# Kernel optimization log

Measured on AMD Instinct MI355X. Metric: run time of the kernel, lower is better.

The kernel has to match this reference:

```python
import jax, jax.numpy as jnp
import numpy as np

B, H, S, DH = 1, 16, 4096, 64
SPARSITY = 0.1
NEG = -1e9


def setup_inputs() -> dict:
    key = jax.random.key(0)
    kq, kk, kv, kp, km = jax.random.split(key, 5)
    query = jax.random.normal(kq, (B, H, S, DH), dtype=jnp.float32)
    k_ = jax.random.normal(kk, (B, H, S, DH), dtype=jnp.float32)
    v_ = jax.random.normal(kv, (B, H, S, DH), dtype=jnp.float32)
    pat = jax.random.uniform(kp, (S, S)) < SPARSITY
    pat = pat | jnp.eye(S, dtype=bool)
    sparse_pattern = pat[None, None]  # [1,1,S,S]
    mask = jax.random.randint(km, (1, 1, 1, S), 0, 2, dtype=jnp.int32)
    return {"query": query, "key": k_, "value": v_,
            "sparse_pattern": sparse_pattern, "mask": mask}


def reference(query, key, value, sparse_pattern, mask):
    scale = 1.0 / jnp.sqrt(jnp.asarray(DH, dtype=query.dtype))
    # [B,H,S,S] attention scores
    scores = jnp.einsum('bhqd,bhkd->bhqk', query, key) * scale
    scores = jnp.where(sparse_pattern, scores, NEG)
    scores = jnp.where(mask == 0, NEG, scores)
    weights = jax.nn.softmax(scores, axis=-1)
    return jnp.einsum('bhqk,bhkd->bhqd', weights, value)
```

## Files before the change

kernel.cpp:

```cpp
#include <hip/hip_runtime.h>
#include <hip/hip_bf16.h>

#define S_LEN 4096
#define DHD   64
#define NH    16
#define NKT   64
#define KVB   64
#define WQ    32
#define NW    4
#define QB    (WQ * NW)
#define QSCALE 0.18033688011112042f
#define THRS   8.656170245333781f

#if __has_builtin(__builtin_amdgcn_exp2f)
#define EXP2(x) __builtin_amdgcn_exp2f(x)
#else
#define EXP2(x) exp2f(x)
#endif

typedef __bf16 bf16x8 __attribute__((ext_vector_type(8)));
typedef __bf16 bf16x4 __attribute__((ext_vector_type(4)));
typedef float  f32x16 __attribute__((ext_vector_type(16)));
typedef float  f32x4  __attribute__((ext_vector_type(4)));
typedef unsigned u32;
typedef unsigned u32x4v __attribute__((ext_vector_type(4)));
typedef unsigned long long u64;

#define MFMA32 __builtin_amdgcn_mfma_f32_32x32x16_bf16

__device__ __forceinline__ int swz(int row, int col) {
  return row * 64 + ((((col >> 3) ^ (row & 7)) << 3) | (col & 7));
}

__device__ __forceinline__ u32 pk(float a, float b) {
  __bf16 x = (__bf16)a, y = (__bf16)b;
  u32 lo = (u32)__builtin_bit_cast(unsigned short, x);
  u32 hi = (u32)__builtin_bit_cast(unsigned short, y);
  return lo | (hi << 16);
}

__device__ __forceinline__ void gload16(const void* g, void* l) {
  __builtin_amdgcn_global_load_lds((const __attribute__((address_space(1))) void*)g,
                                   (__attribute__((address_space(3))) void*)l, 16, 0, 0);
}

__device__ __forceinline__ void plswap(u32& x, u32& y) {
  asm("v_permlane32_swap_b32 %0, %1" : "+v"(x), "+v"(y));
}

union PAW { u32x4v w; bf16x8 h; };

template <int MODE>
__device__ __forceinline__ bool patget(const void* __restrict__ p, int q, int k) {
  const size_t idx = (size_t)q * S_LEN + k;
  if constexpr (MODE == 1) return ((const unsigned char*)p)[idx] != 0;
  else if constexpr (MODE == 0) return ((const int*)p)[idx] != 0;
  else return ((const float*)p)[idx] != 0.0f;
}

__global__ void __launch_bounds__(256, 2) attn32c(
    const float* __restrict__ Qg, const __bf16* __restrict__ Kc, const __bf16* __restrict__ Vc,
    const u64* __restrict__ packw,
    const int* __restrict__ mask, float* __restrict__ out) {
  __shared__ __align__(16) __bf16 Kls[4][KVB * DHD];
  __shared__ __align__(16) __bf16 Vls[4][DHD * KVB];
  __shared__ float sfb[NW][WQ];
  __shared__ int msum[NW];

  const int gid = (blockIdx.x & 7) * 64 + (blockIdx.x >> 3);
  const int h = gid >> 5;
  const int q0 = (gid & 31) * QB;

  const int t = threadIdx.x, lane = t & 63, wv = t >> 6;
  const int l32 = lane & 31, hi = lane >> 5;
  const int qrow = q0 + wv * WQ + l32;

  int c = 0;
#pragma unroll
  for (int j = 0; j < 16; j++) c += (mask[t * 16 + j] != 0);
#pragma unroll
  for (int d = 1; d < 64; d <<= 1) c += __shfl_xor(c, d);
  if (lane == 0) msum[wv] = c;

  bf16x8 aQ[4];
  {
    const float* qp = Qg + ((size_t)h * S_LEN + qrow) * DHD;
#pragma unroll
    for (int cc = 0; cc < 4; cc++) {
      float4 x = *(const float4*)(qp + cc * 16 + hi * 8);
      float4 y = *(const float4*)(qp + cc * 16 + hi * 8 + 4);
      bf16x8 f;
      f[0] = (__bf16)(x.x * QSCALE); f[1] = (__bf16)(x.y * QSCALE);
      f[2] = (__bf16)(x.z * QSCALE); f[3] = (__bf16)(x.w * QSCALE);
      f[4] = (__bf16)(y.x * QSCALE); f[5] = (__bf16)(y.y * QSCALE);
      f[6] = (__bf16)(y.z * QSCALE); f[7] = (__bf16)(y.w * QSCALE);
      aQ[cc] = f;
    }
  }
  bf16x8 onesf;
#pragma unroll
  for (int j = 0; j < 8; j++) onesf[j] = (__bf16)1.0f;
  f32x16 zv;
#pragma unroll
  for (int r = 0; r < 16; r++) zv[r] = 0.f;

  __syncthreads();
  const int nact = msum[0] + msum[1] + msum[2] + msum[3];
  const int nt = (nact + 63) >> 6;
  const int np = ((nt + 1) & ~1) >> 1;

  const __bf16* Kb = Kc + (size_t)h * NKT * 4096;
  const __bf16* Vb = Vc + (size_t)h * NKT * 4096;

  auto stage = [&](int slot, int kt) {
    const __bf16* kbase = Kb + (size_t)kt * 4096;
    const __bf16* vbase = Vb + (size_t)kt * 4096;
#pragma unroll
    for (int i = 0; i < 2; i++) {
      const int j = wv * 2 + i;
      gload16(kbase + j * 512 + lane * 8, &Kls[slot][j * 512]);
      gload16(vbase + j * 512 + lane * 8, &Vls[slot][j * 512]);
    }
  };

  f32x16 Oc0 = zv, Oc1 = zv, Ol = zv;
  float m_run = -__builtin_inff();
  const u64* prow = packw + qrow;

  __builtin_amdgcn_sched_barrier(0);
  u64 pwA = prow[0];
  u64 pwB = prow[(size_t)1 * S_LEN];
  stage(0, 0);
  stage(1, 1);

  for (int it = 0; it < np; it++) {
    const int buf = (it & 1) << 1;
    u64 pwA_n = 0, pwB_n = 0;
    if (it + 1 < np) {
      pwA_n = prow[(size_t)(2 * it + 2) * S_LEN];
      pwB_n = prow[(size_t)(2 * it + 3) * S_LEN];
      stage(buf ^ 2, 2 * it + 2);
      stage((buf ^ 2) + 1, 2 * it + 3);
      asm volatile("s_waitcnt vmcnt(10)" ::: "memory");
    } else {
      asm volatile("s_waitcnt vmcnt(0)" ::: "memory");
    }
    __builtin_amdgcn_s_barrier();
    __builtin_amdgcn_sched_barrier(0);

    const __bf16* KlA = Kls[buf];
    const __bf16* KlB = Kls[buf + 1];
    const __bf16* VlA = Vls[buf];
    const __bf16* VlB = Vls[buf + 1];

    f32x16 pA0, pA1, pB0, pB1;
    __builtin_amdgcn_s_setprio(1);
#pragma unroll
    for (int cc = 0; cc < 4; cc++) {
      const int g = (((2 * cc + hi) ^ (l32 & 7)) << 3);
      const bf16x8 kA0 = *(const bf16x8*)&KlA[l32 * 64 + g];
      const bf16x8 kA1 = *(const bf16x8*)&KlA[(32 + l32) * 64 + g];
      const bf16x8 kB0 = *(const bf16x8*)&KlB[l32 * 64 + g];
      const bf16x8 kB1 = *(const bf16x8*)&KlB[(32 + l32) * 64 + g];
      pA0 = MFMA32(kA0, aQ[cc], cc ? pA0 : zv, 0, 0, 0);
      pA1 = MFMA32(kA1, aQ[cc], cc ? pA1 : zv, 0, 0, 0);
      pB0 = MFMA32(kB0, aQ[cc], cc ? pB0 : zv, 0, 0, 0);
      pB1 = MFMA32(kB1, aQ[cc], cc ? pB1 : zv, 0, 0, 0);
    }
    __builtin_amdgcn_s_setprio(0);

    float mx[32];
#pragma unroll
    for (int i = 0; i < 8; i++) {
      mx[i]      = fmaxf(pA0[2 * i], pA0[2 * i + 1]);
      mx[8 + i]  = fmaxf(pA1[2 * i], pA1[2 * i + 1]);
      mx[16 + i] = fmaxf(pB0[2 * i], pB0[2 * i + 1]);
      mx[24 + i] = fmaxf(pB1[2 * i], pB1[2 * i + 1]);
    }
#pragma unroll
    for (int s = 16; s >= 1; s >>= 1)
#pragma unroll
      for (int i = 0; i < s; i++) mx[i] = fmaxf(mx[i], mx[i + s]);
    const float pm = fmaxf(mx[0], __shfl_xor(mx[0], 32));

    if (!__all(pm <= m_run + THRS)) {
      const float mn = fmaxf(m_run, pm);
      const float sf = EXP2(m_run - mn);
      m_run = mn;
      if (lane < 32) sfb[wv][l32] = sf;
#pragma unroll
      for (int rq = 0; rq < 4; rq++) {
        const f32x4 s4 = *(const f32x4*)&sfb[wv][rq * 8 + 4 * hi];
#pragma unroll
        for (int rr = 0; rr < 4; rr++) {
          Oc0[rq * 4 + rr] *= s4[rr];
          Oc1[rq * 4 + rr] *= s4[rr];
          Ol[rq * 4 + rr]  *= s4[rr];
        }
      }
    }

    const u32 a0b = (u32)pwA, a1b = (u32)(pwA >> 32);
    const u32 wA0 = hi ? ((a0b >> 4) | (a1b << 28)) : a0b;
    const u32 wA1 = hi ? (a1b >> 4) : a1b;
    const u32 b0b = (u32)pwB, b1b = (u32)(pwB >> 32);
    const u32 wB0 = hi ? ((b0b >> 4) | (b1b << 28)) : b0b;
    const u32 wB1 = hi ? (b1b >> 4) : b1b;

#pragma unroll
    for (int r = 0; r < 16; r++) {
      const int sp = (r & 3) + 8 * (r >> 2);
      float eA0 = EXP2(pA0[r] - m_run);
      float eA1 = EXP2(pA1[r] - m_run);
      float eB0 = EXP2(pB0[r] - m_run);
      float eB1 = EXP2(pB1[r] - m_run);
      const int tA0 = (int)(wA0 << (31 - sp)) >> 31;
      const int tA1 = (int)(wA1 << (31 - sp)) >> 31;
      const int tB0 = (int)(wB0 << (31 - sp)) >> 31;
      const int tB1 = (int)(wB1 << (31 - sp)) >> 31;
      pA0[r] = __uint_as_float(__float_as_uint(eA0) & (u32)tA0);
      pA1[r] = __uint_as_float(__float_as_uint(eA1) & (u32)tA1);
      pB0[r] = __uint_as_float(__float_as_uint(eB0) & (u32)tB0);
      pB1[r] = __uint_as_float(__float_as_uint(eB1) & (u32)tB1);
    }

    __builtin_amdgcn_s_setprio(1);
#pragma unroll
    for (int ks = 0; ks < 4; ks++) {
      const f32x16& ps = (ks < 2) ? pA0 : pA1;
      const int b = (ks & 1) * 8;
      u32 x0 = pk(ps[b + 0], ps[b + 1]), x1 = pk(ps[b + 2], ps[b + 3]);
      u32 y0 = pk(ps[b + 4], ps[b + 5]), y1 = pk(ps[b + 6], ps[b + 7]);
      plswap(x0, y0);
      plswap(x1, y1);
      PAW pa;
      pa.w = (u32x4v){x0, x1, y0, y1};
      const int g = (((2 * ks + hi) ^ (l32 & 7)) << 3);
      const bf16x8 v0 = *(const bf16x8*)&VlA[l32 * 64 + g];
      const bf16x8 v1 = *(const bf16x8*)&VlA[(32 + l32) * 64 + g];
      Oc0 = MFMA32(pa.h, v0, Oc0, 0, 0, 0);
      Oc1 = MFMA32(pa.h, v1, Oc1, 0, 0, 0);
      Ol  = MFMA32(pa.h, onesf, Ol, 0, 0, 0);
    }
#pragma unroll
    for (int ks = 0; ks < 4; ks++) {
      const f32x16& ps = (ks < 2) ? pB0 : pB1;
      const int b = (ks & 1) * 8;
      u32 x0 = pk(ps[b + 0], ps[b + 1]), x1 = pk(ps[b + 2], ps[b + 3]);
      u32 y0 = pk(ps[b + 4], ps[b + 5]), y1 = pk(ps[b + 6], ps[b + 7]);
      plswap(x0, y0);
      plswap(x1, y1);
      PAW pa;
      pa.w = (u32x4v){x0, x1, y0, y1};
      const int g = (((2 * ks + hi) ^ (l32 & 7)) << 3);
      const bf16x8 v0 = *(const bf16x8*)&VlB[l32 * 64 + g];
      const bf16x8 v1 = *(const bf16x8*)&VlB[(32 + l32) * 64 + g];
      Oc0 = MFMA32(pa.h, v0, Oc0, 0, 0, 0);
      Oc1 = MFMA32(pa.h, v1, Oc1, 0, 0, 0);
      Ol  = MFMA32(pa.h, onesf, Ol, 0, 0, 0);
    }
    __builtin_amdgcn_s_setprio(0);

    __builtin_amdgcn_s_barrier();
    pwA = pwA_n;
    pwB = pwB_n;
  }

  float* ob = out + ((size_t)h * S_LEN + q0 + wv * WQ) * DHD;
#pragma unroll
  for (int rq = 0; rq < 4; rq++) {
#pragma unroll
    for (int rr = 0; rr < 4; rr++) {
      const int r = rq * 4 + rr;
      const float linv = 1.0f / Ol[r];
      const int qq = rr + 8 * rq + 4 * hi;
      ob[(size_t)qq * DHD + l32]      = Oc0[r] * linv;
      ob[(size_t)qq * DHD + 32 + l32] = Oc1[r] * linv;
    }
  }
}

__global__ void __launch_bounds__(256) prep_all(
    const unsigned* __restrict__ pat32, const int* __restrict__ mask,
    const float* __restrict__ K, const float* __restrict__ V,
    u64* __restrict__ packw, __bf16* __restrict__ Kc, __bf16* __restrict__ Vc) {
  __shared__ int idxs[S_LEN];
  __shared__ int red8[8];
  __shared__ __align__(16) unsigned rowbuf[4096];
  const int t = threadIdx.x, lane = t & 63, wv = t >> 6;

  unsigned mb = 0;
#pragma unroll
  for (int j = 0; j < 16; j++) mb |= (unsigned)(mask[t * 16 + j] != 0) << j;
  const int cnt = __builtin_popcount(mb);
  int inc = cnt;
  for (int d = 1; d < 64; d <<= 1) {
    const int v = __shfl_up(inc, d);
    if (lane >= d) inc += v;
  }
  if (lane == 63) red8[wv] = inc;
  __syncthreads();
  int base = 0;
  for (int w = 0; w < wv; w++) base += red8[w];
  const int nact = red8[0] + red8[1] + red8[2] + red8[3];
  int pfx = base + inc - cnt;
#pragma unroll
  for (int j = 0; j < 16; j++)
    if ((mb >> j) & 1) idxs[pfx++] = t * 16 + j;
  __syncthreads();
  const int nt = (nact + 63) >> 6;
  const int nte = (nt + 1) & ~1;

  if (blockIdx.x < S_LEN) {
    const int q = blockIdx.x;
    unsigned acc = 0;
    for (int i = t; i < 4096; i += 256) {
      const unsigned w = pat32[i];
      if (w == 0x3F800000u) acc |= 2u;
      else if (w & 0xFFFFFF00u) acc |= 1u;
    }
    for (int d = 1; d < 64; d <<= 1) acc |= (unsigned)__shfl_xor((int)acc, d);
    if (lane == 0) red8[4 + wv] = (int)acc;
    __syncthreads();
    acc = (unsigned)(red8[4] | red8[5] | red8[6] | red8[7]);
    const int mode = (acc & 2u) ? 2 : ((acc & 1u) ? 1 : 0);

    if (mode == 1) {
      const uint4* src = (const uint4*)((const unsigned char*)pat32 + ((size_t)q << 12));
      ((uint4*)rowbuf)[t] = src[t];
    } else {
      const uint4* src = (const uint4*)(pat32 + ((size_t)q << 12));
#pragma unroll
      for (int i = 0; i < 4; i++) ((uint4*)rowbuf)[t + 256 * i] = src[t + 256 * i];
    }
    __syncthreads();
    const unsigned char* rb = (const unsigned char*)rowbuf;
    const int nkw = nte * 64;
    for (int bs = 0; bs < nkw; bs += 256) {
      const int j = bs + t;
      bool pb = false;
      if (j < nact) {
        const int k = idxs[j];
        pb = (mode == 1) ? (rb[k] != 0) : (rowbuf[k] != 0);
      }
      const u64 b = __ballot(pb);
      if ((t & 63) == 0) packw[(size_t)(j >> 6) * S_LEN + q] = b;
    }
  } else {
    const int bb = blockIdx.x - S_LEN;
    const int kt = bb & 63, h = bb >> 6;
    if (kt >= nte) return;
    __bf16* Kd = Kc + ((size_t)(h * NKT + kt)) * 4096;
    __bf16* Vd = Vc + ((size_t)(h * NKT + kt)) * 4096;
    const float* Kb = K + (size_t)h * S_LEN * DHD;
    const float* Vb = V + (size_t)h * S_LEN * DHD;
#pragma unroll
    for (int i = 0; i < 4; i++) {
      const int u = t + 256 * i;
      const int kk = u >> 4, d = (u & 15) * 4;
      const int kg = kt * 64 + kk;
      float4 v = {0.f, 0.f, 0.f, 0.f};
      if (kg < nact) v = *(const float4*)(Kb + (size_t)idxs[kg] * DHD + d);
      bf16x4 b;
      b[0] = (__bf16)v.x; b[1] = (__bf16)v.y; b[2] = (__bf16)v.z; b[3] = (__bf16)v.w;
      *(bf16x4*)&Kd[swz(kk, d)] = b;
    }
#pragma unroll
    for (int i = 0; i < 2; i++) {
      const int u = t + 256 * i;
      const int kp = u & 31, d4 = u >> 5;
      const int g0 = kt * 64 + 2 * kp, g1 = g0 + 1;
      float4 a = {0.f, 0.f, 0.f, 0.f}, b = {0.f, 0.f, 0.f, 0.f};
      if (g0 < nact) a = *(const float4*)(Vb + (size_t)idxs[g0] * DHD + d4 * 4);
      if (g1 < nact) b = *(const float4*)(Vb + (size_t)idxs[g1] * DHD + d4 * 4);
      const float* A = reinterpret_cast<const float*>(&a);
      const float* B = reinterpret_cast<const float*>(&b);
#pragma unroll
      for (int j = 0; j < 4; j++) {
        *(u32*)&Vd[swz(d4 * 4 + j, 2 * kp)] = pk(A[j], B[j]);
      }
    }
  }
}

template <bool PACKED, int MODE>
__global__ void __launch_bounds__(256, 2) attn32(
    const float* __restrict__ Qg, const float* __restrict__ Kg, const float* __restrict__ Vg,
    const u64* __restrict__ packw, const void* __restrict__ pat, const int* __restrict__ mask,
    float* __restrict__ out) {
  __shared__ __align__(16) __bf16 Kls[2][KVB * DHD];
  __shared__ __align__(16) __bf16 Vls[2][DHD * KVB];
  __shared__ float sfb[NW][WQ];
  const int gid = (blockIdx.x & 7) * 64 + (blockIdx.x >> 3);
  const int h = gid >> 5;
  const int q0 = (gid & 31) * QB;
  const int t = threadIdx.x, lane = t & 63, wv = t >> 6;
  const int l32 = lane & 31, hi = lane >> 5;
  const int qrow = q0 + wv * WQ + l32;
  bf16x8 aQ[4];
  {
    const float* qp = Qg + ((size_t)h * S_LEN + qrow) * DHD;
#pragma unroll
    for (int cc = 0; cc < 4; cc++) {
      float4 x = *(const float4*)(qp + cc * 16 + hi * 8);
      float4 y = *(const float4*)(qp + cc * 16 + hi * 8 + 4);
      bf16x8 f;
      f[0] = (__bf16)(x.x * QSCALE); f[1] = (__bf16)(x.y * QSCALE);
      f[2] = (__bf16)(x.z * QSCALE); f[3] = (__bf16)(x.w * QSCALE);
      f[4] = (__bf16)(y.x * QSCALE); f[5] = (__bf16)(y.y * QSCALE);
      f[6] = (__bf16)(y.z * QSCALE); f[7] = (__bf16)(y.w * QSCALE);
      aQ[cc] = f;
    }
  }
  const float* Kb = Kg + (size_t)h * S_LEN * DHD;
  const float* Vb = Vg + (size_t)h * S_LEN * DHD;
  float4 kreg[4], vreg0[2], vreg1[2];
  auto issue_loads = [&](int kt) {
    const float* kbase = Kb + (size_t)kt * KVB * DHD;
    const float* vbase = Vb + (size_t)kt * KVB * DHD;
#pragma unroll
    for (int i = 0; i < 4; i++) {
      const int u = t + 256 * i;
      kreg[i] = *(const float4*)(kbase + (size_t)(u >> 4) * DHD + (u & 15) * 4);
    }
#pragma unroll
    for (int i = 0; i < 2; i++) {
      const int u = t + 256 * i;
      const int kp = u & 31, d4 = u >> 5;
      vreg0[i] = *(const float4*)(vbase + (size_t)(2 * kp) * DHD + d4 * 4);
      vreg1[i] = *(const float4*)(vbase + (size_t)(2 * kp + 1) * DHD + d4 * 4);
    }
  };
  auto write_tile = [&](int buf) {
    __bf16* Kd = Kls[buf];
    __bf16* Vd = Vls[buf];
#pragma unroll
    for (int i = 0; i < 4; i++) {
      const int u = t + 256 * i;
      const int kk = u >> 4, d = (u & 15) * 4;
      const float4 v = kreg[i];
      bf16x4 b;
      b[0] = (__bf16)v.x; b[1] = (__bf16)v.y; b[2] = (__bf16)v.z; b[3] = (__bf16)v.w;
      *(bf16x4*)&Kd[swz(kk, d)] = b;
    }
#pragma unroll
    for (int i = 0; i < 2; i++) {
      const int u = t + 256 * i;
      const int kp = u & 31, d4 = u >> 5;
      const float* A = reinterpret_cast<const float*>(&vreg0[i]);
      const float* B = reinterpret_cast<const float*>(&vreg1[i]);
#pragma unroll
      for (int j = 0; j < 4; j++) {
        *(u32*)&Vd[swz(d4 * 4 + j, 2 * kp)] = pk(A[j], B[j]);
      }
    }
  };
  f32x16 Oc0, Oc1;
#pragma unroll
  for (int r = 0; r < 16; r++) { Oc0[r] = 0.f; Oc1[r] = 0.f; }
  float m_run = -__builtin_inff(), l_run = 0.f;
  const u64* prow = PACKED ? (packw + qrow) : nullptr;
  issue_loads(0);
  write_tile(0);
  __syncthreads();
  int cur = 0;
  for (int kt = 0; kt < NKT; kt++) {
    if (kt + 1 < NKT) issue_loads(kt + 1);
    u64 pw;
    if constexpr (PACKED) {
      pw = prow[(size_t)kt * S_LEN];
    } else {
      pw = 0;
      for (int j = 0; j < 64; j++) {
        const bool pb = patget<MODE>(pat, qrow, kt * 64 + j) && (mask[kt * 64 + j] != 0);
        pw |= (u64)pb << j;
      }
    }
    const __bf16* Kl = Kls[cur];
    f32x16 p0, p1;
#pragma unroll
    for (int r = 0; r < 16; r++) { p0[r] = 0.f; p1[r] = 0.f; }
#pragma unroll
    for (int cc = 0; cc < 4; cc++) {
      const int g = (((2 * cc + hi) ^ (l32 & 7)) << 3);
      const bf16x8 k0 = *(const bf16x8*)&Kl[l32 * 64 + g];
      const bf16x8 k1 = *(const bf16x8*)&Kl[(32 + l32) * 64 + g];
      p0 = MFMA32(k0, aQ[cc], p0, 0, 0, 0);
      p1 = MFMA32(k1, aQ[cc], p1, 0, 0, 0);
    }
    float pm = p0[0];
#pragma unroll
    for (int r = 1; r < 16; r++) pm = fmaxf(pm, p0[r]);
#pragma unroll
    for (int r = 0; r < 16; r++) pm = fmaxf(pm, p1[r]);
    pm = fmaxf(pm, __shfl_xor(pm, 32));
    if (!__all(pm <= m_run + THRS)) {
      const float mn = fmaxf(m_run, pm);
      const float sf = EXP2(m_run - mn);
      m_run = mn;
      l_run *= sf;
      if (lane < 32) sfb[wv][l32] = sf;
#pragma unroll
      for (int rq = 0; rq < 4; rq++) {
        const f32x4 s4 = *(const f32x4*)&sfb[wv][rq * 8 + 4 * hi];
#pragma unroll
        for (int rr = 0; rr < 4; rr++) {
          Oc0[rq * 4 + rr] *= s4[rr];
          Oc1[rq * 4 + rr] *= s4[rr];
        }
      }
    }
    const u32 b0 = (u32)pw, b1 = (u32)(pw >> 32);
    const u32 w0 = hi ? ((b0 >> 4) | (b1 << 28)) : b0;
    const u32 w1 = hi ? (b1 >> 4) : b1;
    float ls = 0.f;
#pragma unroll
    for (int r = 0; r < 16; r++) {
      const int sp = (r & 3) + 8 * (r >> 2);
      float e0 = EXP2(p0[r] - m_run);
      float e1 = EXP2(p1[r] - m_run);
      const int t0 = (int)(w0 << (31 - sp)) >> 31;
      const int t1 = (int)(w1 << (31 - sp)) >> 31;
      e0 = __uint_as_float(__float_as_uint(e0) & (u32)t0);
      e1 = __uint_as_float(__float_as_uint(e1) & (u32)t1);
      p0[r] = e0; p1[r] = e1;
      ls += e0 + e1;
    }
    ls += __shfl_xor(ls, 32);
    l_run += ls;
    const __bf16* Vl = Vls[cur];
#pragma unroll
    for (int ks = 0; ks < 4; ks++) {
      const f32x16& ps = (ks < 2) ? p0 : p1;
      const int b = (ks & 1) * 8;
      u32 x0 = pk(ps[b + 0], ps[b + 1]), x1 = pk(ps[b + 2], ps[b + 3]);
      u32 y0 = pk(ps[b + 4], ps[b + 5]), y1 = pk(ps[b + 6], ps[b + 7]);
      plswap(x0, y0);
      plswap(x1, y1);
      PAW pa;
      pa.w = (u32x4v){x0, x1, y0, y1};
      const int g = (((2 * ks + hi) ^ (l32 & 7)) << 3);
      const bf16x8 v0 = *(const bf16x8*)&Vl[l32 * 64 + g];
      const bf16x8 v1 = *(const bf16x8*)&Vl[(32 + l32) * 64 + g];
      Oc0 = MFMA32(pa.h, v0, Oc0, 0, 0, 0);
      Oc1 = MFMA32(pa.h, v1, Oc1, 0, 0, 0);
    }
    if (kt + 1 < NKT) write_tile(cur ^ 1);
    __syncthreads();
    cur ^= 1;
  }
  const float linv = 1.0f / l_run;
  if (lane < 32) sfb[wv][l32] = linv;
  __syncthreads();
  float* ob = out + ((size_t)h * S_LEN + q0 + wv * WQ) * DHD;
#pragma unroll
  for (int rq = 0; rq < 4; rq++) {
    const f32x4 s4 = *(const f32x4*)&sfb[wv][rq * 8 + 4 * hi];
#pragma unroll
    for (int rr = 0; rr < 4; rr++) {
      const int r = rq * 4 + rr;
      const int qq = rr + 8 * rq + 4 * hi;
      ob[(size_t)qq * DHD + l32]      = Oc0[r] * s4[rr];
      ob[(size_t)qq * DHD + 32 + l32] = Oc1[r] * s4[rr];
    }
  }
}

__global__ void detect_kernel(const unsigned* __restrict__ p, int* __restrict__ flag) {
  __shared__ unsigned red[256];
  const int t = threadIdx.x;
  unsigned acc = 0;
  for (int i = t; i < 16384; i += 256) {
    const unsigned w = p[i];
    if (w == 0x3F800000u) acc |= 2u;
    else if (w & 0xFFFFFF00u) acc |= 1u;
  }
  red[t] = acc;
  __syncthreads();
  if (t == 0) {
    unsigned a = 0;
    for (int i = 0; i < 256; i++) a |= red[i];
    flag[0] = (a & 2u) ? 2 : ((a & 1u) ? 1 : 0);
  }
}

__global__ void pack_mask_kernel(const int* __restrict__ mask, u64* __restrict__ maskw) {
  const int w = threadIdx.x;
  u64 m = 0;
  for (int j = 0; j < 64; j++) m |= (u64)(mask[(w << 6) + j] != 0) << j;
  maskw[w] = m;
}

__global__ void pack_pat_kernel(const void* __restrict__ pat, const u64* __restrict__ maskw,
                                u64* __restrict__ packw, const int* __restrict__ flagp) {
  const int gid = blockIdx.x * 256 + threadIdx.x;
  const int q = gid >> 6, w = gid & 63;
  const int mode = flagp[0];
  u64 bits = 0;
  if (mode == 1) {
    const u64* p = (const u64*)((const unsigned char*)pat + ((size_t)q << 12) + (w << 6));
#pragma unroll
    for (int c = 0; c < 8; c++) {
      u64 v = p[c];
      v |= v >> 4; v |= v >> 2; v |= v >> 1;
      v &= 0x0101010101010101ull;
      bits |= ((v * 0x0102040810204080ull) >> 56) << (c * 8);
    }
  } else if (mode == 0) {
    const int4* p = (const int4*)((const int*)pat + ((size_t)q << 12) + ((size_t)w << 6));
#pragma unroll
    for (int c = 0; c < 16; c++) {
      const int4 x = p[c];
      bits |= (u64)(x.x != 0) << (c * 4);
      bits |= (u64)(x.y != 0) << (c * 4 + 1);
      bits |= (u64)(x.z != 0) << (c * 4 + 2);
      bits |= (u64)(x.w != 0) << (c * 4 + 3);
    }
  } else {
    const float4* p = (const float4*)((const float*)pat + ((size_t)q << 12) + ((size_t)w << 6));
#pragma unroll
    for (int c = 0; c < 16; c++) {
      const float4 x = p[c];
      bits |= (u64)(x.x != 0.0f) << (c * 4);
      bits |= (u64)(x.y != 0.0f) << (c * 4 + 1);
      bits |= (u64)(x.z != 0.0f) << (c * 4 + 2);
      bits |= (u64)(x.w != 0.0f) << (c * 4 + 3);
    }
  }
  packw[(size_t)w * S_LEN + q] = bits & maskw[w];
}

extern "C" void kernel_launch(void* const* d_in, const int* in_sizes, int n_in,
                              void* d_out, int out_size, void* d_ws, size_t ws_size,
                              hipStream_t stream) {
  (void)in_sizes; (void)n_in; (void)out_size;
  const float* Q  = (const float*)d_in[0];
  const float* K  = (const float*)d_in[1];
  const float* V  = (const float*)d_in[2];
  const void* pat = d_in[3];
  const int* mask = (const int*)d_in[4];
  float* out      = (float*)d_out;

  const size_t FLAG_OFF  = 0;
  const size_t MASKW_OFF = 24576;
  const size_t PACKW_OFF = 32768;
  const size_t KC_OFF    = PACKW_OFF + (size_t)S_LEN * NKT * 8;
  const size_t VC_OFF    = KC_OFF + (size_t)NH * NKT * 4096 * 2;
  const size_t NEED_FULL = VC_OFF + (size_t)NH * NKT * 4096 * 2;
  const size_t NEED_MID  = PACKW_OFF + (size_t)S_LEN * NKT * 8;

  const dim3 grid(32 * NH, 1);

  if (ws_size >= NEED_FULL) {
    u64* packw = (u64*)((char*)d_ws + PACKW_OFF);
    __bf16* Kc = (__bf16*)((char*)d_ws + KC_OFF);
    __bf16* Vc = (__bf16*)((char*)d_ws + VC_OFF);
    prep_all<<<S_LEN + NKT * NH, 256, 0, stream>>>((const unsigned*)pat, mask, K, V,
                                                   packw, Kc, Vc);
    attn32c<<<grid, 256, 0, stream>>>(Q, Kc, Vc, packw, mask, out);
  } else if (ws_size >= NEED_MID) {
    int* flag  = (int*)((char*)d_ws + FLAG_OFF);
    u64* maskw = (u64*)((char*)d_ws + MASKW_OFF);
    u64* packw = (u64*)((char*)d_ws + PACKW_OFF);
    detect_kernel<<<1, 256, 0, stream>>>((const unsigned*)pat, flag);
    pack_mask_kernel<<<1, 64, 0, stream>>>(mask, maskw);
    pack_pat_kernel<<<(S_LEN * 64) / 256, 256, 0, stream>>>(pat, maskw, packw, flag);
    attn32<true, 0><<<grid, 256, 0, stream>>>(Q, K, V, packw, pat, mask, out);
  } else {
    attn32<false, 1><<<grid, 256, 0, stream>>>(Q, K, V, nullptr, pat, mask, out);
  }
}
```

Measured before the change: 95.40 us.

## Split KV tiles across two wave groups per block with LDS merge

The attention kernel now launches 512 threads per block. The eight waves form two groups of four, each processing alternating KV tiles for the same 128 query rows with its own double buffer. At the end, group 1 writes its partial O, row sums and running max to shared memory, and group 0 merges them with max-rescaling before the final normalisation. This doubles wave-level parallelism per query block to hide latency and shortens each wave's serial KV loop. The cost is an extra LDS reduction, higher register and LDS pressure (launch bounds now ask for 512 threads and 4 waves per EU), and less work per iteration to overlap loads.

```diff
diff --git a/kernel.cpp b/kernel.cpp
--- a/kernel.cpp
+++ b/kernel.cpp
@@ -7,8 +7,7 @@
 #define NKT   64
 #define KVB   64
 #define WQ    32
-#define NW    4
-#define QB    (WQ * NW)
+#define QB    128
 #define QSCALE 0.18033688011112042f
 #define THRS   8.656170245333781f
 
@@ -58,26 +57,28 @@
   else return ((const float*)p)[idx] != 0.0f;
 }
 
-__global__ void __launch_bounds__(256, 2) attn32c(
+__global__ void __launch_bounds__(512, 4) attn32c(
     const float* __restrict__ Qg, const __bf16* __restrict__ Kc, const __bf16* __restrict__ Vc,
     const u64* __restrict__ packw,
     const int* __restrict__ mask, float* __restrict__ out) {
-  __shared__ __align__(16) __bf16 Kls[4][KVB * DHD];
-  __shared__ __align__(16) __bf16 Vls[4][DHD * KVB];
-  __shared__ float sfb[NW][WQ];
-  __shared__ int msum[NW];
+  __shared__ __align__(16) char smem[65536];
+  __shared__ float sfb[8][WQ];
+  __shared__ int msum[8];
+  __bf16* Kls = (__bf16*)smem;
+  __bf16* Vls = (__bf16*)(smem + 32768);
 
   const int gid = (blockIdx.x & 7) * 64 + (blockIdx.x >> 3);
   const int h = gid >> 5;
   const int q0 = (gid & 31) * QB;
 
   const int t = threadIdx.x, lane = t & 63, wv = t >> 6;
+  const int grp = wv >> 2, ws = wv & 3;
   const int l32 = lane & 31, hi = lane >> 5;
-  const int qrow = q0 + wv * WQ + l32;
+  const int qrow = q0 + ws * WQ + l32;
 
   int c = 0;
 #pragma unroll
-  for (int j = 0; j < 16; j++) c += (mask[t * 16 + j] != 0);
+  for (int j = 0; j < 8; j++) c += (mask[t * 8 + j] != 0);
 #pragma unroll
   for (int d = 1; d < 64; d <<= 1) c += __shfl_xor(c, d);
   if (lane == 0) msum[wv] = c;
@@ -105,21 +106,25 @@
   for (int r = 0; r < 16; r++) zv[r] = 0.f;
 
   __syncthreads();
-  const int nact = msum[0] + msum[1] + msum[2] + msum[3];
+  int nact = 0;
+#pragma unroll
+  for (int w = 0; w < 8; w++) nact += msum[w];
   const int nt = (nact + 63) >> 6;
-  const int np = ((nt + 1) & ~1) >> 1;
+  const int nte = (nt + 1) & ~1;
+  const int nh = nte >> 1;
 
   const __bf16* Kb = Kc + (size_t)h * NKT * 4096;
   const __bf16* Vb = Vc + (size_t)h * NKT * 4096;
 
-  auto stage = [&](int slot, int kt) {
+  auto stage = [&](int buf, int kt) {
     const __bf16* kbase = Kb + (size_t)kt * 4096;
     const __bf16* vbase = Vb + (size_t)kt * 4096;
+    const int s = (grp * 2 + buf) * 4096;
 #pragma unroll
     for (int i = 0; i < 2; i++) {
-      const int j = wv * 2 + i;
-      gload16(kbase + j * 512 + lane * 8, &Kls[slot][j * 512]);
-      gload16(vbase + j * 512 + lane * 8, &Vls[slot][j * 512]);
+      const int j = ws * 2 + i;
+      gload16(kbase + j * 512 + lane * 8, &Kls[s + j * 512]);
+      gload16(vbase + j * 512 + lane * 8, &Vls[s + j * 512]);
     }
   };
 
@@ -128,57 +133,46 @@
   const u64* prow = packw + qrow;
 
   __builtin_amdgcn_sched_barrier(0);
-  u64 pwA = prow[0];
-  u64 pwB = prow[(size_t)1 * S_LEN];
-  stage(0, 0);
-  stage(1, 1);
-
-  for (int it = 0; it < np; it++) {
-    const int buf = (it & 1) << 1;
-    u64 pwA_n = 0, pwB_n = 0;
-    if (it + 1 < np) {
-      pwA_n = prow[(size_t)(2 * it + 2) * S_LEN];
-      pwB_n = prow[(size_t)(2 * it + 3) * S_LEN];
-      stage(buf ^ 2, 2 * it + 2);
-      stage((buf ^ 2) + 1, 2 * it + 3);
-      asm volatile("s_waitcnt vmcnt(10)" ::: "memory");
+  u64 pw = prow[(size_t)grp * S_LEN];
+  u64 pw_n = 0;
+  stage(0, grp);
+  int buf = 0;
+
+  for (int it = 0; it < nh; it++) {
+    if (it + 1 < nh) {
+      const int ktn = 2 * it + 2 + grp;
+      pw_n = prow[(size_t)ktn * S_LEN];
+      stage(buf ^ 1, ktn);
+      asm volatile("s_waitcnt vmcnt(5)" ::: "memory");
     } else {
       asm volatile("s_waitcnt vmcnt(0)" ::: "memory");
     }
     __builtin_amdgcn_s_barrier();
     __builtin_amdgcn_sched_barrier(0);
 
-    const __bf16* KlA = Kls[buf];
-    const __bf16* KlB = Kls[buf + 1];
-    const __bf16* VlA = Vls[buf];
-    const __bf16* VlB = Vls[buf + 1];
-
-    f32x16 pA0, pA1, pB0, pB1;
+    const __bf16* Kl = &Kls[(grp * 2 + buf) * 4096];
+    const __bf16* Vl = &Vls[(grp * 2 + buf) * 4096];
+
+    f32x16 p0, p1;
     __builtin_amdgcn_s_setprio(1);
 #pragma unroll
     for (int cc = 0; cc < 4; cc++) {
       const int g = (((2 * cc + hi) ^ (l32 & 7)) << 3);
-      const bf16x8 kA0 = *(const bf16x8*)&KlA[l32 * 64 + g];
-      const bf16x8 kA1 = *(const bf16x8*)&KlA[(32 + l32) * 64 + g];
-      const bf16x8 kB0 = *(const bf16x8*)&KlB[l32 * 64 + g];
-      const bf16x8 kB1 = *(const bf16x8*)&KlB[(32 + l32) * 64 + g];
-      pA0 = MFMA32(kA0, aQ[cc], cc ? pA0 : zv, 0, 0, 0);
-      pA1 = MFMA32(kA1, aQ[cc], cc ? pA1 : zv, 0, 0, 0);
-      pB0 = MFMA32(kB0, aQ[cc], cc ? pB0 : zv, 0, 0, 0);
-      pB1 = MFMA32(kB1, aQ[cc], cc ? pB1 : zv, 0, 0, 0);
+      const bf16x8 k0 = *(const bf16x8*)&Kl[l32 * 64 + g];
+      const bf16x8 k1 = *(const bf16x8*)&Kl[(32 + l32) * 64 + g];
+      p0 = MFMA32(k0, aQ[cc], cc ? p0 : zv, 0, 0, 0);
+      p1 = MFMA32(k1, aQ[cc], cc ? p1 : zv, 0, 0, 0);
     }
     __builtin_amdgcn_s_setprio(0);
 
-    float mx[32];
+    float mx[16];
 #pragma unroll
     for (int i = 0; i < 8; i++) {
-      mx[i]      = fmaxf(pA0[2 * i], pA0[2 * i + 1]);
-      mx[8 + i]  = fmaxf(pA1[2 * i], pA1[2 * i + 1]);
-      mx[16 + i] = fmaxf(pB0[2 * i], pB0[2 * i + 1]);
-      mx[24 + i] = fmaxf(pB1[2 * i], pB1[2 * i + 1]);
-    }
-#pragma unroll
-    for (int s = 16; s >= 1; s >>= 1)
+      mx[i]     = fmaxf(p0[2 * i], p0[2 * i + 1]);
+      mx[8 + i] = fmaxf(p1[2 * i], p1[2 * i + 1]);
+    }
+#pragma unroll
+    for (int s = 8; s >= 1; s >>= 1)
 #pragma unroll
       for (int i = 0; i < s; i++) mx[i] = fmaxf(mx[i], mx[i + s]);
     const float pm = fmaxf(mx[0], __shfl_xor(mx[0], 32));
@@ -200,34 +194,25 @@
       }
     }
 
-    const u32 a0b = (u32)pwA, a1b = (u32)(pwA >> 32);
-    const u32 wA0 = hi ? ((a0b >> 4) | (a1b << 28)) : a0b;
-    const u32 wA1 = hi ? (a1b >> 4) : a1b;
-    const u32 b0b = (u32)pwB, b1b = (u32)(pwB >> 32);
-    const u32 wB0 = hi ? ((b0b >> 4) | (b1b << 28)) : b0b;
-    const u32 wB1 = hi ? (b1b >> 4) : b1b;
+    const u32 b0 = (u32)pw, b1 = (u32)(pw >> 32);
+    const u32 w0 = hi ? ((b0 >> 4) | (b1 << 28)) : b0;
+    const u32 w1 = hi ? (b1 >> 4) : b1;
 
 #pragma unroll
     for (int r = 0; r < 16; r++) {
       const int sp = (r & 3) + 8 * (r >> 2);
-      float eA0 = EXP2(pA0[r] - m_run);
-      float eA1 = EXP2(pA1[r] - m_run);
-      float eB0 = EXP2(pB0[r] - m_run);
-      float eB1 = EXP2(pB1[r] - m_run);
-      const int tA0 = (int)(wA0 << (31 - sp)) >> 31;
-      const int tA1 = (int)(wA1 << (31 - sp)) >> 31;
-      const int tB0 = (int)(wB0 << (31 - sp)) >> 31;
-      const int tB1 = (int)(wB1 << (31 - sp)) >> 31;
-      pA0[r] = __uint_as_float(__float_as_uint(eA0) & (u32)tA0);
-      pA1[r] = __uint_as_float(__float_as_uint(eA1) & (u32)tA1);
-      pB0[r] = __uint_as_float(__float_as_uint(eB0) & (u32)tB0);
-      pB1[r] = __uint_as_float(__float_as_uint(eB1) & (u32)tB1);
+      float e0 = EXP2(p0[r] - m_run);
+      float e1 = EXP2(p1[r] - m_run);
+      const int t0 = (int)(w0 << (31 - sp)) >> 31;
+      const int t1 = (int)(w1 << (31 - sp)) >> 31;
+      p0[r] = __uint_as_float(__float_as_uint(e0) & (u32)t0);
+      p1[r] = __uint_as_float(__float_as_uint(e1) & (u32)t1);
     }
 
     __builtin_amdgcn_s_setprio(1);
 #pragma unroll
     for (int ks = 0; ks < 4; ks++) {
-      const f32x16& ps = (ks < 2) ? pA0 : pA1;
+      const f32x16& ps = (ks < 2) ? p0 : p1;
       const int b = (ks & 1) * 8;
       u32 x0 = pk(ps[b + 0], ps[b + 1]), x1 = pk(ps[b + 2], ps[b + 3]);
       u32 y0 = pk(ps[b + 4], ps[b + 5]), y1 = pk(ps[b + 6], ps[b + 7]);
@@ -236,46 +221,49 @@
       PAW pa;
       pa.w = (u32x4v){x0, x1, y0, y1};
       const int g = (((2 * ks + hi) ^ (l32 & 7)) << 3);
-      const bf16x8 v0 = *(const bf16x8*)&VlA[l32 * 64 + g];
-      const bf16x8 v1 = *(const bf16x8*)&VlA[(32 + l32) * 64 + g];
+      const bf16x8 v0 = *(const bf16x8*)&Vl[l32 * 64 + g];
+      const bf16x8 v1 = *(const bf16x8*)&Vl[(32 + l32) * 64 + g];
       Oc0 = MFMA32(pa.h, v0, Oc0, 0, 0, 0);
       Oc1 = MFMA32(pa.h, v1, Oc1, 0, 0, 0);
       Ol  = MFMA32(pa.h, onesf, Ol, 0, 0, 0);
     }
-#pragma unroll
-    for (int ks = 0; ks < 4; ks++) {
-      const f32x16& ps = (ks < 2) ? pB0 : pB1;
-      const int b = (ks & 1) * 8;
-      u32 x0 = pk(ps[b + 0], ps[b + 1]), x1 = pk(ps[b + 2], ps[b + 3]);
-      u32 y0 = pk(ps[b + 4], ps[b + 5]), y1 = pk(ps[b + 6], ps[b + 7]);
-      plswap(x0, y0);
-      plswap(x1, y1);
-      PAW pa;
-      pa.w = (u32x4v){x0, x1, y0, y1};
-      const int g = (((2 * ks + hi) ^ (l32 & 7)) << 3);
-      const bf16x8 v0 = *(const bf16x8*)&VlB[l32 * 64 + g];
-      const bf16x8 v1 = *(const bf16x8*)&VlB[(32 + l32) * 64 + g];
-      Oc0 = MFMA32(pa.h, v0, Oc0, 0, 0, 0);
-      Oc1 = MFMA32(pa.h, v1, Oc1, 0, 0, 0);
-      Ol  = MFMA32(pa.h, onesf, Ol, 0, 0, 0);
-    }
     __builtin_amdgcn_s_setprio(0);
 
     __builtin_amdgcn_s_barrier();
-    pwA = pwA_n;
-    pwB = pwB_n;
-  }
-
-  float* ob = out + ((size_t)h * S_LEN + q0 + wv * WQ) * DHD;
-#pragma unroll
-  for (int rq = 0; rq < 4; rq++) {
-#pragma unroll
-    for (int rr = 0; rr < 4; rr++) {
-      const int r = rq * 4 + rr;
-      const float linv = 1.0f / Ol[r];
-      const int qq = rr + 8 * rq + 4 * hi;
-      ob[(size_t)qq * DHD + l32]      = Oc0[r] * linv;
-      ob[(size_t)qq * DHD + 32 + l32] = Oc1[r] * linv;
+    buf ^= 1;
+    pw = pw_n;
+  }
+
+  float* cbuf = (float*)smem;
+  float* cb = cbuf + (ws * 64 + lane) * 49;
+  if (grp == 1) {
+#pragma unroll
+    for (int r = 0; r < 16; r++) {
+      cb[r] = Oc0[r]; cb[16 + r] = Oc1[r]; cb[32 + r] = Ol[r];
+    }
+    if (lane < 32) sfb[4 + ws][l32] = m_run;
+  } else {
+    if (lane < 32) sfb[ws][l32] = m_run;
+  }
+  __syncthreads();
+  if (grp == 0) {
+    float* ob = out + ((size_t)h * S_LEN + q0 + ws * WQ) * DHD;
+#pragma unroll
+    for (int rq = 0; rq < 4; rq++) {
+      const f32x4 a4 = *(const f32x4*)&sfb[ws][rq * 8 + 4 * hi];
+      const f32x4 b4 = *(const f32x4*)&sfb[4 + ws][rq * 8 + 4 * hi];
+#pragma unroll
+      for (int rr = 0; rr < 4; rr++) {
+        const int r = rq * 4 + rr;
+        const float mm = fmaxf(a4[rr], b4[rr]);
+        const float sa = EXP2(a4[rr] - mm);
+        const float sb = EXP2(b4[rr] - mm);
+        const float den = Ol[r] * sa + cb[32 + r] * sb;
+        const float linv = 1.0f / den;
+        const int qq = rr + 8 * rq + 4 * hi;
+        ob[(size_t)qq * DHD + l32]      = (Oc0[r] * sa + cb[r] * sb) * linv;
+        ob[(size_t)qq * DHD + 32 + l32] = (Oc1[r] * sa + cb[16 + r] * sb) * linv;
+      }
     }
   }
 }
@@ -390,7 +378,7 @@
     float* __restrict__ out) {
   __shared__ __align__(16) __bf16 Kls[2][KVB * DHD];
   __shared__ __align__(16) __bf16 Vls[2][DHD * KVB];
-  __shared__ float sfb[NW][WQ];
+  __shared__ float sfb[4][WQ];
   const int gid = (blockIdx.x & 7) * 64 + (blockIdx.x >> 3);
   const int h = gid >> 5;
   const int q0 = (gid & 31) * QB;
@@ -657,7 +645,7 @@
     __bf16* Vc = (__bf16*)((char*)d_ws + VC_OFF);
     prep_all<<<S_LEN + NKT * NH, 256, 0, stream>>>((const unsigned*)pat, mask, K, V,
                                                    packw, Kc, Vc);
-    attn32c<<<grid, 256, 0, stream>>>(Q, Kc, Vc, packw, mask, out);
+    attn32c<<<grid, 512, 0, stream>>>(Q, Kc, Vc, packw, mask, out);
   } else if (ws_size >= NEED_MID) {
     int* flag  = (int*)((char*)d_ws + FLAG_OFF);
     u64* maskw = (u64*)((char*)d_ws + MASKW_OFF);
```

Result: slower. 123.2 us (+29.1%).
